# Optimization experiments

Hardware: AMD Instinct MI355X
Metric: run time of the kernel (lower is better)

Reference implementation:

```python
import jax, jax.numpy as jnp
import numpy as np

N = 20000       # nodes
E = 320000      # edges (before self-loops)
F_IN = 128
HID = 128
HEADS = 4
OUT_DIM = 2
B = 64          # graphs in batch
SLOPE = 0.2     # GATv2 leaky_relu negative slope (PyG default)


def _glorot(key, shape):
    fan_in, fan_out = shape[0], shape[1]
    limit = np.sqrt(6.0 / (fan_in + fan_out)).astype(np.float32)
    return jax.random.uniform(key, shape, jnp.float32, -limit, limit)


def setup_inputs() -> dict:
    key = jax.random.key(0)
    ks = jax.random.split(key, 24)
    inp = {
        'x': jax.random.normal(ks[0], (N, F_IN), jnp.float32),
        'edge_src': jax.random.randint(ks[1], (E,), 0, N),
        'edge_dst': jax.random.randint(ks[2], (E,), 0, N),
        'batch': jnp.sort(jax.random.randint(ks[3], (N,), 0, B)),
        # layer 1: in=F_IN, out=HEADS*HID, concat
        'Wl1': _glorot(ks[4], (F_IN, HEADS * HID)),
        'Wr1': _glorot(ks[5], (F_IN, HEADS * HID)),
        'bl1': jnp.zeros((HEADS * HID,), jnp.float32),
        'br1': jnp.zeros((HEADS * HID,), jnp.float32),
        'att1': _glorot(ks[6], (HEADS, HID)),
        'bias1': jnp.zeros((HEADS * HID,), jnp.float32),
        # layer 2: in=HEADS*HID, out=HEADS*HID, concat
        'Wl2': _glorot(ks[7], (HEADS * HID, HEADS * HID)),
        'Wr2': _glorot(ks[8], (HEADS * HID, HEADS * HID)),
        'bl2': jnp.zeros((HEADS * HID,), jnp.float32),
        'br2': jnp.zeros((HEADS * HID,), jnp.float32),
        'att2': _glorot(ks[9], (HEADS, HID)),
        'bias2': jnp.zeros((HEADS * HID,), jnp.float32),
        # layer 3: in=HEADS*HID, heads=1, concat=False -> out=HID
        'Wl3': _glorot(ks[10], (HEADS * HID, HID)),
        'Wr3': _glorot(ks[11], (HEADS * HID, HID)),
        'bl3': jnp.zeros((HID,), jnp.float32),
        'br3': jnp.zeros((HID,), jnp.float32),
        'att3': _glorot(ks[12], (1, HID)),
        'bias3': jnp.zeros((HID,), jnp.float32),
        # output MLP
        'W_mlp1': _glorot(ks[13], (HID, HID)),
        'b_mlp1': jnp.zeros((HID,), jnp.float32),
        'W_mlp2': _glorot(ks[14], (HID, OUT_DIM)),
        'b_mlp2': jnp.zeros((OUT_DIM,), jnp.float32),
    }
    return inp


def gatv2_layer(x, src, dst, Wl, Wr, bl, br, att, bias, concat):
    """PyG GATv2Conv (eval mode): alpha_ij = softmax_j over N(i) of a^T LeakyReLU(xl_j + xr_i)."""
    H, C = att.shape
    n = x.shape[0]
    xl = (x @ Wl + bl).reshape(n, H, C)   # source transform
    e = jax.nn.leaky_relu(xl[src] + (x @ Wr + br).reshape(n, H, C)[dst], SLOPE)  # [E,H,C]
    logits = jnp.einsum('ehc,hc->eh', e, att)                                    # [E,H]
    # segment softmax over destination node
    m = jax.ops.segment_max(logits, dst, num_segments=n)
    alpha = jnp.exp(logits - m[dst])
    denom = jax.ops.segment_sum(alpha, dst, num_segments=n)
    alpha = alpha / denom[dst]
    out = jax.ops.segment_sum(xl[src] * alpha[..., None], dst, num_segments=n)   # [N,H,C]
    out = out.reshape(n, H * C) if concat else out.mean(axis=1)
    return out + bias


def reference(x, edge_src, edge_dst, batch,
              Wl1, Wr1, bl1, br1, att1, bias1,
              Wl2, Wr2, bl2, br2, att2, bias2,
              Wl3, Wr3, bl3, br3, att3, bias3,
              W_mlp1, b_mlp1, W_mlp2, b_mlp2):
    n = x.shape[0]
    loop = jnp.arange(n, dtype=edge_src.dtype)
    src = jnp.concatenate([edge_src, loop])   # PyG add_self_loops=True
    dst = jnp.concatenate([edge_dst, loop])

    h = jax.nn.elu(gatv2_layer(x, src, dst, Wl1, Wr1, bl1, br1, att1, bias1, True))
    h = jax.nn.elu(gatv2_layer(h, src, dst, Wl2, Wr2, bl2, br2, att2, bias2, True))
    h = jax.nn.elu(gatv2_layer(h, src, dst, Wl3, Wr3, bl3, br3, att3, bias3, False))

    # global_mean_pool over graph ids
    counts = jnp.maximum(jax.ops.segment_sum(jnp.ones((n,), h.dtype), batch, num_segments=B), 1.0)
    pooled = jax.ops.segment_sum(h, batch, num_segments=B) / counts[:, None]

    hidden = jax.nn.relu(pooled @ W_mlp1 + b_mlp1)
    return hidden @ W_mlp2 + b_mlp2
```

## Files before the change

### kernel.cpp

```cpp
#include <hip/hip_runtime.h>
#include <math.h>


typedef __attribute__((ext_vector_type(4))) float f32x4;
typedef __attribute__((ext_vector_type(8))) _Float16 f16x8;
typedef __attribute__((ext_vector_type(4))) _Float16 f16x4;
typedef __attribute__((ext_vector_type(2))) _Float16 f16x2;

__device__ __forceinline__ float elu1(float x) {
    return (x > 0.f) ? x : (__expf(x) - 1.f);
}
__device__ __forceinline__ f16x2 pk_leaky(f16x2 s) {
    const f16x2 slope = {(_Float16)0.2f, (_Float16)0.2f};
    return __builtin_elementwise_max(s, s * slope);
}

__device__ __forceinline__ float dpp_sum16(float v) {
    int t;
    t = __builtin_amdgcn_mov_dpp(__float_as_int(v), 0xB1, 0xF, 0xF, true);
    v += __int_as_float(t);
    t = __builtin_amdgcn_mov_dpp(__float_as_int(v), 0x4E, 0xF, 0xF, true);
    v += __int_as_float(t);
    t = __builtin_amdgcn_mov_dpp(__float_as_int(v), 0x141, 0xF, 0xF, true);
    v += __int_as_float(t);
    t = __builtin_amdgcn_mov_dpp(__float_as_int(v), 0x140, 0xF, 0xF, true);
    v += __int_as_float(t);
    return v;
}

__global__ void zero32_kernel(int* __restrict__ p, int n) {
    int i = blockIdx.x * 256 + threadIdx.x;
    if (i < n) p[i] = 0;
}

__global__ void count_kernel(const int* __restrict__ dst, int* __restrict__ cnt,
                             int E, int N) {
    int e = blockIdx.x * 256 + threadIdx.x;
    if (e < E + N) {
        int d = (e < E) ? dst[e] : (e - E);
        atomicAdd(&cnt[d], 1);
    }
}

__global__ __launch_bounds__(256) void scan1_kernel(const int* __restrict__ cnt,
                                                    int* __restrict__ psum, int N) {
    __shared__ int red[256];
    int idx = blockIdx.x * 256 + threadIdx.x;
    red[threadIdx.x] = (idx < N) ? cnt[idx] : 0;
    __syncthreads();
    for (int s = 128; s > 0; s >>= 1) {
        if (threadIdx.x < s) red[threadIdx.x] += red[threadIdx.x + s];
        __syncthreads();
    }
    if (threadIdx.x == 0) psum[blockIdx.x] = red[0];
}
__global__ void scan2_kernel(int* __restrict__ psum, int nch) {
    if (threadIdx.x == 0) {
        int run = 0;
        for (int i = 0; i < nch; ++i) { int v = psum[i]; psum[i] = run; run += v; }
    }
}
__global__ __launch_bounds__(256) void scan3_kernel(const int* __restrict__ cnt,
                                                    const int* __restrict__ psum,
                                                    int* __restrict__ rowstart,
                                                    int* __restrict__ cursor, int N) {
    __shared__ int buf[256];
    int idx = blockIdx.x * 256 + threadIdx.x;
    int v = (idx < N) ? cnt[idx] : 0;
    buf[threadIdx.x] = v;
    __syncthreads();
    for (int off = 1; off < 256; off <<= 1) {
        int t = (threadIdx.x >= off) ? buf[threadIdx.x - off] : 0;
        __syncthreads();
        buf[threadIdx.x] += t;
        __syncthreads();
    }
    int excl = buf[threadIdx.x] - v + psum[blockIdx.x];
    if (idx < N) {
        rowstart[idx] = excl;
        cursor[idx]   = excl;
        if (idx == N - 1) rowstart[N] = excl + v;
    }
}

__global__ void scatter_kernel(const int* __restrict__ src, const int* __restrict__ dst,
                               int* __restrict__ cursor, int* __restrict__ csr_src,
                               int E, int N) {
    int e = blockIdx.x * 256 + threadIdx.x;
    if (e < E + N) {
        int d, s;
        if (e < E) { d = dst[e]; s = src[e]; }
        else       { d = e - E; s = e - E; }
        int pos = atomicAdd(&cursor[d], 1);
        csr_src[pos] = s;
    }
}

__global__ void boundary_kernel(const int* __restrict__ batch,
                                int* __restrict__ gstart, int N, int B) {
    int n = blockIdx.x * 256 + threadIdx.x;
    if (n > N) return;
    int cur  = (n < N) ? batch[n] : B;
    int prev = (n == 0) ? -1 : batch[n - 1];
    for (int g = prev + 1; g <= cur; ++g) gstart[g] = n;
}

__global__ void convA_kernel(const float* __restrict__ X, _Float16* __restrict__ A,
                             int n_valid, int n_total) {
    int i = (blockIdx.x * 256 + threadIdx.x) * 4;
    if (i >= n_total) return;
    float4 v = (i < n_valid) ? *(const float4*)(X + i) : make_float4(0.f, 0.f, 0.f, 0.f);
    f16x4 h;
    h.x = (_Float16)v.x; h.y = (_Float16)v.y;
    h.z = (_Float16)v.z; h.w = (_Float16)v.w;
    *(f16x4*)(A + i) = h;
}

__global__ __launch_bounds__(256) void convWT_kernel(
    const float* __restrict__ Wl, const float* __restrict__ Wr,
    _Float16* __restrict__ Bth, _Float16* __restrict__ Btl, int K, int Nh) {
    __shared__ float tile[32][33];
    int kb = blockIdx.x * 32;
    int nb = blockIdx.y * 32;
    int tx = threadIdx.x;
    int ty = threadIdx.y;
#pragma unroll
    for (int j = 0; j < 4; ++j) {
        int kk = kb + ty + j * 8;
        int nn = nb + tx;
        float v = (nn < Nh) ? Wl[(size_t)kk * Nh + nn]
                            : Wr[(size_t)kk * Nh + (nn - Nh)];
        tile[ty + j * 8][tx] = v;
    }
    __syncthreads();
#pragma unroll
    for (int j = 0; j < 4; ++j) {
        int nn = nb + ty + j * 8;
        int kk = kb + tx;
        float v = tile[tx][ty + j * 8];
        _Float16 h = (_Float16)v;
        Bth[(size_t)nn * K + kk] = h;
        Btl[(size_t)nn * K + kk] = (_Float16)(v - (float)h);
    }
}

#define SCW 132
__global__ __launch_bounds__(256, 1) void gemm_f16_kernel(
    const _Float16* __restrict__ A,
    const _Float16* __restrict__ Bh, const _Float16* __restrict__ Bl,
    const float* __restrict__ biasL, const float* __restrict__ biasR, int Nh_,
    _Float16* __restrict__ P, _Float16* __restrict__ Q, int K, int NT) {
    __shared__ __align__(16) char smem[49152];
    float* sC = (float*)(smem);

    const int tid  = threadIdx.x;
    const int lane = tid & 63;
    const int wv   = tid >> 6;
    const int wm   = wv & 1;
    const int wn   = wv >> 1;
    const int fm   = lane & 15;
    const int q    = lane >> 4;

    const int bi = blockIdx.x;
    const int kx = bi & 7;
    const int tt = bi >> 3;
    const int m0 = ((tt / NT) * 8 + kx) * 128;
    const int n0 = (tt % NT) * 128;

    const int r0  = lane >> 2;
    const int kco = (lane & 3) << 3;

    f32x4 acc[4][4];
#pragma unroll
    for (int i = 0; i < 4; ++i)
#pragma unroll
        for (int j = 0; j < 4; ++j) {
            acc[i][j].x = 0.f; acc[i][j].y = 0.f;
            acc[i][j].z = 0.f; acc[i][j].w = 0.f;
        }

    const int nIters = K >> 5;
    int cur = 0;
    {
        char* base = smem;
#pragma unroll
        for (int j = 0; j < 2; ++j) {
            int wc  = wv * 2 + j;
            int row = wc * 16 + r0;
            size_t ga = (size_t)(m0 + row) * K + kco;
            size_t gb = (size_t)(n0 + row) * K + kco;
            int lofs = wc * 1024;
            __builtin_amdgcn_global_load_lds(
                (const __attribute__((address_space(1))) void*)(A + ga),
                (__attribute__((address_space(3))) void*)(base + lofs), 16, 0, 0);
            __builtin_amdgcn_global_load_lds(
                (const __attribute__((address_space(1))) void*)(Bh + gb),
                (__attribute__((address_space(3))) void*)(base + 8192 + lofs), 16, 0, 0);
            __builtin_amdgcn_global_load_lds(
                (const __attribute__((address_space(1))) void*)(Bl + gb),
                (__attribute__((address_space(3))) void*)(base + 16384 + lofs), 16, 0, 0);
        }
    }
    for (int it = 0; it < nIters; ++it) {
        __syncthreads();
        if (it + 1 < nIters) {
            char* base = smem + (cur ^ 1) * 24576;
            int ks = (it + 1) << 5;
#pragma unroll
            for (int j = 0; j < 2; ++j) {
                int wc  = wv * 2 + j;
                int row = wc * 16 + r0;
                size_t ga = (size_t)(m0 + row) * K + ks + kco;
                size_t gb = (size_t)(n0 + row) * K + ks + kco;
                int lofs = wc * 1024;
                __builtin_amdgcn_global_load_lds(
                    (const __attribute__((address_space(1))) void*)(A + ga),
                    (__attribute__((address_space(3))) void*)(base + lofs), 16, 0, 0);
                __builtin_amdgcn_global_load_lds(
                    (const __attribute__((address_space(1))) void*)(Bh + gb),
                    (__attribute__((address_space(3))) void*)(base + 8192 + lofs), 16, 0, 0);
                __builtin_amdgcn_global_load_lds(
                    (const __attribute__((address_space(1))) void*)(Bl + gb),
                    (__attribute__((address_space(3))) void*)(base + 16384 + lofs), 16, 0, 0);
            }
        }

        _Float16* cA  = (_Float16*)(smem + cur * 24576);
        _Float16* cBh = (_Float16*)(smem + cur * 24576 + 8192);
        _Float16* cBl = (_Float16*)(smem + cur * 24576 + 16384);
        f16x8 ah[4];
#pragma unroll
        for (int mi = 0; mi < 4; ++mi)
            ah[mi] = *(const f16x8*)&cA[(wm * 64 + mi * 16 + fm) * 32 + q * 8];
#pragma unroll
        for (int ni = 0; ni < 4; ++ni) {
            int r = (wn * 64 + ni * 16 + fm) * 32 + q * 8;
            f16x8 bh = *(const f16x8*)&cBh[r];
            f16x8 bl = *(const f16x8*)&cBl[r];
#pragma unroll
            for (int mi = 0; mi < 4; ++mi) {
                acc[mi][ni] = __builtin_amdgcn_mfma_f32_16x16x32_f16(ah[mi], bh, acc[mi][ni], 0, 0, 0);
                acc[mi][ni] = __builtin_amdgcn_mfma_f32_16x16x32_f16(ah[mi], bl, acc[mi][ni], 0, 0, 0);
            }
        }
        cur ^= 1;
    }

    float bsv[4];
#pragma unroll
    for (int ni = 0; ni < 4; ++ni) {
        int col = n0 + wn * 64 + ni * 16 + fm;
        bsv[ni] = (col < Nh_) ? biasL[col] : biasR[col - Nh_];
    }

    _Float16* dstbase = (n0 < Nh_) ? P : Q;
    const int col0 = (n0 < Nh_) ? n0 : (n0 - Nh_);

#pragma unroll
    for (int c = 0; c < 2; ++c) {
        __syncthreads();
        if (wm == c) {
#pragma unroll
            for (int mi = 0; mi < 4; ++mi)
#pragma unroll
                for (int ni = 0; ni < 4; ++ni) {
                    int base = (mi * 16 + q * 4) * SCW + wn * 64 + ni * 16 + fm;
                    sC[base]           = acc[mi][ni].x + bsv[ni];
                    sC[base + SCW]     = acc[mi][ni].y + bsv[ni];
                    sC[base + 2 * SCW] = acc[mi][ni].z + bsv[ni];
                    sC[base + 3 * SCW] = acc[mi][ni].w + bsv[ni];
                }
        }
        __syncthreads();
#pragma unroll
        for (int j = 0; j < 8; ++j) {
            int flat = j * 256 + tid;
            int row  = flat >> 5;
            int col  = (flat & 31) * 4;
            f32x4 v = *(const f32x4*)(sC + row * SCW + col);
            f16x4 hv;
            hv.x = (_Float16)v.x; hv.y = (_Float16)v.y;
            hv.z = (_Float16)v.z; hv.w = (_Float16)v.w;
            *(f16x4*)(dstbase + (size_t)(m0 + c * 64 + row) * Nh_ + col0 + col) = hv;
        }
    }
}


__device__ __forceinline__ void edge4_one(
    int s, const _Float16* __restrict__ P, int c0,
    const f16x2* r2, const f16x2* t2, float& l_run, float* acc) {
    f16x8 h = *(const f16x8*)(P + ((size_t)s << 9) + c0);
    float p = 0.f;
#pragma unroll
    for (int k = 0; k < 4; ++k) {
        f16x2 a; a.x = h[2 * k]; a.y = h[2 * k + 1];
        p = __builtin_amdgcn_fdot2(pk_leaky(a + r2[k]), t2[k], p, false);
    }
    p = dpp_sum16(p);
    float w = __expf(p);
    l_run += w;
#pragma unroll
    for (int j = 0; j < 8; ++j)
        acc[j] = fmaf((float)h[j], w, acc[j]);
}

__global__ __launch_bounds__(256) void gat_edge4_kernel(
    const _Float16* __restrict__ P, const _Float16* __restrict__ Q,
    const float* __restrict__ att, const float* __restrict__ bias,
    const int* __restrict__ rowstart, const int* __restrict__ srcs,
    _Float16* __restrict__ H, int N) {
    int wv = threadIdx.x >> 6;
    int lane = threadIdx.x & 63;
    int n = blockIdx.x * 4 + wv;
    if (n >= N) return;
    int c0 = lane * 8;

    f16x8 rv = *(const f16x8*)(Q + (size_t)n * 512 + c0);
    f16x2 r2[4], t2[4];
#pragma unroll
    for (int k = 0; k < 4; ++k) {
        r2[k].x = rv[2 * k]; r2[k].y = rv[2 * k + 1];
        t2[k].x = (_Float16)att[c0 + 2 * k];
        t2[k].y = (_Float16)att[c0 + 2 * k + 1];
    }

    float acc[8];
#pragma unroll
    for (int j = 0; j < 8; ++j) acc[j] = 0.f;
    float l_run = 0.f;

    int beg = __builtin_amdgcn_readfirstlane(rowstart[n]);
    int end = __builtin_amdgcn_readfirstlane(rowstart[n + 1]);

    int i = beg;
    int s0 = srcs[i], s1 = srcs[i + 1], s2 = srcs[i + 2], s3 = srcs[i + 3];

    for (; i + 3 < end; ) {
        int f0 = srcs[i + 4], f1 = srcs[i + 5], f2 = srcs[i + 6], f3 = srcs[i + 7];
        int u0 = __builtin_amdgcn_readfirstlane(s0);
        int u1 = __builtin_amdgcn_readfirstlane(s1);
        int u2 = __builtin_amdgcn_readfirstlane(s2);
        int u3 = __builtin_amdgcn_readfirstlane(s3);
        f16x8 h0 = *(const f16x8*)(P + ((size_t)u0 << 9) + c0);
        f16x8 h1 = *(const f16x8*)(P + ((size_t)u1 << 9) + c0);
        f16x8 h2 = *(const f16x8*)(P + ((size_t)u2 << 9) + c0);
        f16x8 h3 = *(const f16x8*)(P + ((size_t)u3 << 9) + c0);
        float p0 = 0.f, p1 = 0.f, p2 = 0.f, p3 = 0.f;
#pragma unroll
        for (int k = 0; k < 4; ++k) {
            f16x2 a0; a0.x = h0[2 * k]; a0.y = h0[2 * k + 1];
            f16x2 a1; a1.x = h1[2 * k]; a1.y = h1[2 * k + 1];
            f16x2 a2; a2.x = h2[2 * k]; a2.y = h2[2 * k + 1];
            f16x2 a3; a3.x = h3[2 * k]; a3.y = h3[2 * k + 1];
            p0 = __builtin_amdgcn_fdot2(pk_leaky(a0 + r2[k]), t2[k], p0, false);
            p1 = __builtin_amdgcn_fdot2(pk_leaky(a1 + r2[k]), t2[k], p1, false);
            p2 = __builtin_amdgcn_fdot2(pk_leaky(a2 + r2[k]), t2[k], p2, false);
            p3 = __builtin_amdgcn_fdot2(pk_leaky(a3 + r2[k]), t2[k], p3, false);
        }
        p0 = dpp_sum16(p0);
        p1 = dpp_sum16(p1);
        p2 = dpp_sum16(p2);
        p3 = dpp_sum16(p3);
        float w0 = __expf(p0);
        float w1 = __expf(p1);
        float w2 = __expf(p2);
        float w3 = __expf(p3);
        l_run += (w0 + w1) + (w2 + w3);
#pragma unroll
        for (int j = 0; j < 8; ++j) {
            float a = fmaf((float)h0[j], w0, acc[j]);
            a = fmaf((float)h1[j], w1, a);
            a = fmaf((float)h2[j], w2, a);
            acc[j] = fmaf((float)h3[j], w3, a);
        }
        i += 4; s0 = f0; s1 = f1; s2 = f2; s3 = f3;
    }
    int rem = end - i;
    if (rem > 0) edge4_one(__builtin_amdgcn_readfirstlane(s0), P, c0, r2, t2, l_run, acc);
    if (rem > 1) edge4_one(__builtin_amdgcn_readfirstlane(s1), P, c0, r2, t2, l_run, acc);
    if (rem > 2) edge4_one(__builtin_amdgcn_readfirstlane(s2), P, c0, r2, t2, l_run, acc);

    float inv = 1.f / l_run;
    f16x8 oh;
#pragma unroll
    for (int j = 0; j < 8; ++j)
        oh[j] = (_Float16)elu1(acc[j] * inv + bias[c0 + j]);
    *(f16x8*)(H + (size_t)n * 512 + c0) = oh;
}

__global__ __launch_bounds__(256) void gat_edge1_kernel(
    const _Float16* __restrict__ P, const _Float16* __restrict__ Q,
    const float* __restrict__ att, const float* __restrict__ bias,
    const int* __restrict__ rowstart, const int* __restrict__ srcs,
    float* __restrict__ out, int N) {
    int wv = threadIdx.x >> 6;
    int lane = threadIdx.x & 63;
    int n = blockIdx.x * 4 + wv;
    if (n >= N) return;
    int qd = lane >> 4;
    int lq = lane & 15;
    int c0 = lq * 8;

    f16x8 rv = *(const f16x8*)(Q + (size_t)n * 128 + c0);
    f16x2 r2[4], t2[4];
#pragma unroll
    for (int k = 0; k < 4; ++k) {
        r2[k].x = rv[2 * k]; r2[k].y = rv[2 * k + 1];
        t2[k].x = (_Float16)att[c0 + 2 * k];
        t2[k].y = (_Float16)att[c0 + 2 * k + 1];
    }

    float acc[8];
#pragma unroll
    for (int j = 0; j < 8; ++j) acc[j] = 0.f;
    float l_run = 0.f;

    int beg = __builtin_amdgcn_readfirstlane(rowstart[n]);
    int end = __builtin_amdgcn_readfirstlane(rowstart[n + 1]);
    for (int e = beg + qd; e < end; e += 4) {
        int s = srcs[e];
        f16x8 hv = *(const f16x8*)(P + ((size_t)s << 7) + c0);
        float p = 0.f;
#pragma unroll
        for (int k = 0; k < 4; ++k) {
            f16x2 a; a.x = hv[2 * k]; a.y = hv[2 * k + 1];
            p = __builtin_amdgcn_fdot2(pk_leaky(a + r2[k]), t2[k], p, false);
        }
        p = dpp_sum16(p);
        float w = __expf(p);
        l_run += w;
#pragma unroll
        for (int j = 0; j < 8; ++j)
            acc[j] = fmaf((float)hv[j], w, acc[j]);
    }
    l_run += __shfl_xor(l_run, 16, 64);
    l_run += __shfl_xor(l_run, 32, 64);
#pragma unroll
    for (int j = 0; j < 8; ++j) {
        acc[j] += __shfl_xor(acc[j], 16, 64);
        acc[j] += __shfl_xor(acc[j], 32, 64);
    }
    float inv = 1.f / l_run;
    int cw = c0 + qd * 2;
    float2 w2;
    w2.x = elu1(acc[qd * 2]     * inv + bias[cw]);
    w2.y = elu1(acc[qd * 2 + 1] * inv + bias[cw + 1]);
    *(float2*)(out + (size_t)n * 128 + cw) = w2;
}

__global__ __launch_bounds__(256) void pool2_kernel(
    const float* __restrict__ h3, const int* __restrict__ gstart,
    float* __restrict__ pooled) {
    __shared__ float red[256];
    int g = blockIdx.x;
    int c = threadIdx.x & 127;
    int h = threadIdx.x >> 7;
    int gs = gstart[g], ge = gstart[g + 1];
    float s = 0.f;
    for (int n = gs + h; n < ge; n += 2) s += h3[(size_t)n * 128 + c];
    red[threadIdx.x] = s;
    __syncthreads();
    if (h == 0) {
        float tot = red[c] + red[c + 128];
        float cnt = fmaxf((float)(ge - gs), 1.f);
        pooled[g * 128 + c] = tot / cnt;
    }
}

__global__ __launch_bounds__(128) void mlp_kernel(
    const float* __restrict__ pooled,
    const float* __restrict__ W1, const float* __restrict__ b1,
    const float* __restrict__ W2, const float* __restrict__ b2,
    float* __restrict__ out) {
    __shared__ float pr[128];
    __shared__ float2 red[128];
    int g = blockIdx.x;
    int t = threadIdx.x;
    pr[t] = pooled[g * 128 + t];
    __syncthreads();
    float h = b1[t];
#pragma unroll 4
    for (int k = 0; k < 128; ++k) h = fmaf(pr[k], W1[k * 128 + t], h);
    h = fmaxf(h, 0.0f);
    red[t] = make_float2(h * W2[t * 2], h * W2[t * 2 + 1]);
    __syncthreads();
    for (int s = 64; s > 0; s >>= 1) {
        if (t < s) {
            red[t].x += red[t + s].x;
            red[t].y += red[t + s].y;
        }
        __syncthreads();
    }
    if (t == 0) {
        out[g * 2]     = red[0].x + b2[0];
        out[g * 2 + 1] = red[0].y + b2[1];
    }
}

extern "C" void kernel_launch(void* const* d_in, const int* in_sizes, int n_in,
                              void* d_out, int out_size, void* d_ws, size_t ws_size,
                              hipStream_t stream) {
    const float* x     = (const float*)d_in[0];
    const int*   esrc  = (const int*)d_in[1];
    const int*   edst  = (const int*)d_in[2];
    const int*   batch = (const int*)d_in[3];
    const float* Wl1   = (const float*)d_in[4];
    const float* Wr1   = (const float*)d_in[5];
    const float* bl1   = (const float*)d_in[6];
    const float* br1   = (const float*)d_in[7];
    const float* att1  = (const float*)d_in[8];
    const float* bias1 = (const float*)d_in[9];
    const float* Wl2   = (const float*)d_in[10];
    const float* Wr2   = (const float*)d_in[11];
    const float* bl2   = (const float*)d_in[12];
    const float* br2   = (const float*)d_in[13];
    const float* att2  = (const float*)d_in[14];
    const float* bias2 = (const float*)d_in[15];
    const float* Wl3   = (const float*)d_in[16];
    const float* Wr3   = (const float*)d_in[17];
    const float* bl3   = (const float*)d_in[18];
    const float* br3   = (const float*)d_in[19];
    const float* att3  = (const float*)d_in[20];
    const float* bias3 = (const float*)d_in[21];
    const float* Wm1   = (const float*)d_in[22];
    const float* bm1   = (const float*)d_in[23];
    const float* Wm2   = (const float*)d_in[24];
    const float* bm2   = (const float*)d_in[25];

    int N  = in_sizes[0] / 128;
    int E  = in_sizes[1];
    int ET = E + N;
    int B  = out_size / 2;
    const int Mp = 160 * 128;
    int nch = (N + 255) / 256;

    char* ws = (char*)d_ws;
    size_t off = 0;
    auto alloc = [&](size_t bytes) -> void* {
        void* p = ws + off;
        off += (bytes + 255) & ~(size_t)255;
        return p;
    };
    _Float16* P    = (_Float16*)alloc((size_t)Mp * 512 * 2);
    _Float16* Q    = (_Float16*)alloc((size_t)Mp * 512 * 2);
    _Float16* A1   = (_Float16*)alloc((size_t)Mp * 128 * 2);
    _Float16* Hb   = (_Float16*)alloc((size_t)Mp * 512 * 2);
    _Float16* Wth1 = (_Float16*)alloc((size_t)1024 * 128 * 2);
    _Float16* Wtl1 = (_Float16*)alloc((size_t)1024 * 128 * 2);
    _Float16* Wth2 = (_Float16*)alloc((size_t)1024 * 512 * 2);
    _Float16* Wtl2 = (_Float16*)alloc((size_t)1024 * 512 * 2);
    _Float16* Wth3 = (_Float16*)alloc((size_t)256 * 512 * 2);
    _Float16* Wtl3 = (_Float16*)alloc((size_t)256 * 512 * 2);
    float*    R3   = (float*)alloc((size_t)Mp * 128 * 4);
    int*    cnt      = (int*)alloc((size_t)N * 4);
    int*    psum     = (int*)alloc((size_t)(nch + 1) * 4);
    int*    rowstart = (int*)alloc((size_t)(N + 1) * 4);
    int*    cursor   = (int*)alloc((size_t)N * 4);
    int*    csr_src  = (int*)alloc((size_t)ET * 4 + 32);
    int*    gstart   = (int*)alloc((size_t)(B + 1) * 4);
    float*  pooled   = (float*)alloc((size_t)B * 128 * 4);
    (void)ws_size;

    zero32_kernel<<<(N + 255) / 256, 256, 0, stream>>>(cnt, N);

    count_kernel<<<(ET + 255) / 256, 256, 0, stream>>>(edst, cnt, E, N);
    scan1_kernel<<<nch, 256, 0, stream>>>(cnt, psum, N);
    scan2_kernel<<<1, 64, 0, stream>>>(psum, nch);
    scan3_kernel<<<nch, 256, 0, stream>>>(cnt, psum, rowstart, cursor, N);
    scatter_kernel<<<(ET + 255) / 256, 256, 0, stream>>>(esrc, edst, cursor, csr_src, E, N);
    boundary_kernel<<<(N + 256) / 256, 256, 0, stream>>>(batch, gstart, N, B);

    convWT_kernel<<<dim3(4, 32),  dim3(32, 8), 0, stream>>>(Wl1, Wr1, Wth1, Wtl1, 128, 512);
    convWT_kernel<<<dim3(16, 32), dim3(32, 8), 0, stream>>>(Wl2, Wr2, Wth2, Wtl2, 512, 512);
    convWT_kernel<<<dim3(16, 8),  dim3(32, 8), 0, stream>>>(Wl3, Wr3, Wth3, Wtl3, 512, 128);

    convA_kernel<<<((Mp * 128 / 4) + 255) / 256, 256, 0, stream>>>(x, A1, N * 128, Mp * 128);

    int eblocks = (N + 3) / 4;

    gemm_f16_kernel<<<160 * 8, 256, 0, stream>>>(A1, Wth1, Wtl1, bl1, br1, 512, P, Q, 128, 8);
    gat_edge4_kernel<<<eblocks, 256, 0, stream>>>(P, Q, att1, bias1, rowstart, csr_src, Hb, N);

    gemm_f16_kernel<<<160 * 8, 256, 0, stream>>>(Hb, Wth2, Wtl2, bl2, br2, 512, P, Q, 512, 8);
    gat_edge4_kernel<<<eblocks, 256, 0, stream>>>(P, Q, att2, bias2, rowstart, csr_src, Hb, N);

    gemm_f16_kernel<<<160 * 2, 256, 0, stream>>>(Hb, Wth3, Wtl3, bl3, br3, 128, P, Q, 512, 2);
    gat_edge1_kernel<<<eblocks, 256, 0, stream>>>(P, Q, att3, bias3, rowstart, csr_src, R3, N);

    pool2_kernel<<<B, 256, 0, stream>>>(R3, gstart, pooled);
    mlp_kernel<<<B, 128, 0, stream>>>(pooled, Wm1, bm1, Wm2, bm2, (float*)d_out);
}
```

Measured before the change: 412.2 us.

## Sort nodes by degree for edge kernels and swizzle GEMM LDS layout

```diff
diff --git a/kernel.cpp b/kernel.cpp
--- a/kernel.cpp
+++ b/kernel.cpp
@@ -105,6 +105,32 @@
     for (int g = prev + 1; g <= cur; ++g) gstart[g] = n;
 }
 
+__global__ void degcnt_kernel(const int* __restrict__ rowstart,
+                              int* __restrict__ dcnt, int N) {
+    int n = blockIdx.x * 256 + threadIdx.x;
+    if (n < N) {
+        int d = rowstart[n + 1] - rowstart[n];
+        d = d < 63 ? d : 63;
+        atomicAdd(&dcnt[d], 1);
+    }
+}
+__global__ void degoff_kernel(const int* __restrict__ dcnt, int* __restrict__ dcur) {
+    if (threadIdx.x == 0) {
+        int run = 0;
+        for (int d = 63; d >= 0; --d) { dcur[d] = run; run += dcnt[d]; }
+    }
+}
+__global__ void degscat_kernel(const int* __restrict__ rowstart,
+                               int* __restrict__ dcur, int* __restrict__ order, int N) {
+    int n = blockIdx.x * 256 + threadIdx.x;
+    if (n < N) {
+        int d = rowstart[n + 1] - rowstart[n];
+        d = d < 63 ? d : 63;
+        int pos = atomicAdd(&dcur[d], 1);
+        order[pos] = n;
+    }
+}
+
 __global__ void convA_kernel(const float* __restrict__ X, _Float16* __restrict__ A,
                              int n_valid, int n_total) {
     int i = (blockIdx.x * 256 + threadIdx.x) * 4;
@@ -160,6 +186,7 @@
     const int wn   = wv >> 1;
     const int fm   = lane & 15;
     const int q    = lane >> 4;
+    const int qa   = q ^ ((fm >> 1) & 3);
 
     const int bi = blockIdx.x;
     const int kx = bi & 7;
@@ -168,7 +195,7 @@
     const int n0 = (tt % NT) * 128;
 
     const int r0  = lane >> 2;
-    const int kco = (lane & 3) << 3;
+    const int kcs = (((lane & 3) ^ ((lane >> 3) & 3)) << 3);
 
     f32x4 acc[4][4];
 #pragma unroll
@@ -187,8 +214,8 @@
         for (int j = 0; j < 2; ++j) {
             int wc  = wv * 2 + j;
             int row = wc * 16 + r0;
-            size_t ga = (size_t)(m0 + row) * K + kco;
-            size_t gb = (size_t)(n0 + row) * K + kco;
+            size_t ga = (size_t)(m0 + row) * K + kcs;
+            size_t gb = (size_t)(n0 + row) * K + kcs;
             int lofs = wc * 1024;
             __builtin_amdgcn_global_load_lds(
                 (const __attribute__((address_space(1))) void*)(A + ga),
@@ -210,8 +237,8 @@
             for (int j = 0; j < 2; ++j) {
                 int wc  = wv * 2 + j;
                 int row = wc * 16 + r0;
-                size_t ga = (size_t)(m0 + row) * K + ks + kco;
-                size_t gb = (size_t)(n0 + row) * K + ks + kco;
+                size_t ga = (size_t)(m0 + row) * K + ks + kcs;
+                size_t gb = (size_t)(n0 + row) * K + ks + kcs;
                 int lofs = wc * 1024;
                 __builtin_amdgcn_global_load_lds(
                     (const __attribute__((address_space(1))) void*)(A + ga),
@@ -231,10 +258,10 @@
         f16x8 ah[4];
 #pragma unroll
         for (int mi = 0; mi < 4; ++mi)
-            ah[mi] = *(const f16x8*)&cA[(wm * 64 + mi * 16 + fm) * 32 + q * 8];
+            ah[mi] = *(const f16x8*)&cA[(wm * 64 + mi * 16 + fm) * 32 + qa * 8];
 #pragma unroll
         for (int ni = 0; ni < 4; ++ni) {
-            int r = (wn * 64 + ni * 16 + fm) * 32 + q * 8;
+            int r = (wn * 64 + ni * 16 + fm) * 32 + qa * 8;
             f16x8 bh = *(const f16x8*)&cBh[r];
             f16x8 bl = *(const f16x8*)&cBl[r];
 #pragma unroll
@@ -290,30 +317,31 @@
 __device__ __forceinline__ void edge4_one(
     int s, const _Float16* __restrict__ P, int c0,
     const f16x2* r2, const f16x2* t2, float& l_run, float* acc) {
-    f16x8 h = *(const f16x8*)(P + ((size_t)s << 9) + c0);
+    union { f16x8 v; f16x2 p[4]; } h;
+    h.v = *(const f16x8*)(P + ((size_t)s << 9) + c0);
     float p = 0.f;
 #pragma unroll
-    for (int k = 0; k < 4; ++k) {
-        f16x2 a; a.x = h[2 * k]; a.y = h[2 * k + 1];
-        p = __builtin_amdgcn_fdot2(pk_leaky(a + r2[k]), t2[k], p, false);
-    }
+    for (int k = 0; k < 4; ++k)
+        p = __builtin_amdgcn_fdot2(pk_leaky(h.p[k] + r2[k]), t2[k], p, false);
     p = dpp_sum16(p);
     float w = __expf(p);
     l_run += w;
 #pragma unroll
     for (int j = 0; j < 8; ++j)
-        acc[j] = fmaf((float)h[j], w, acc[j]);
+        acc[j] = fmaf((float)h.v[j], w, acc[j]);
 }
 
 __global__ __launch_bounds__(256) void gat_edge4_kernel(
     const _Float16* __restrict__ P, const _Float16* __restrict__ Q,
     const float* __restrict__ att, const float* __restrict__ bias,
     const int* __restrict__ rowstart, const int* __restrict__ srcs,
+    const int* __restrict__ order,
     _Float16* __restrict__ H, int N) {
     int wv = threadIdx.x >> 6;
     int lane = threadIdx.x & 63;
-    int n = blockIdx.x * 4 + wv;
-    if (n >= N) return;
+    int idx = blockIdx.x * 4 + wv;
+    if (idx >= N) return;
+    int n = order[idx];
     int c0 = lane * 8;
 
     f16x8 rv = *(const f16x8*)(Q + (size_t)n * 512 + c0);
@@ -342,21 +370,18 @@
         int u1 = __builtin_amdgcn_readfirstlane(s1);
         int u2 = __builtin_amdgcn_readfirstlane(s2);
         int u3 = __builtin_amdgcn_readfirstlane(s3);
-        f16x8 h0 = *(const f16x8*)(P + ((size_t)u0 << 9) + c0);
-        f16x8 h1 = *(const f16x8*)(P + ((size_t)u1 << 9) + c0);
-        f16x8 h2 = *(const f16x8*)(P + ((size_t)u2 << 9) + c0);
-        f16x8 h3 = *(const f16x8*)(P + ((size_t)u3 << 9) + c0);
+        union { f16x8 v; f16x2 p[4]; } h0, h1, h2, h3;
+        h0.v = *(const f16x8*)(P + ((size_t)u0 << 9) + c0);
+        h1.v = *(const f16x8*)(P + ((size_t)u1 << 9) + c0);
+        h2.v = *(const f16x8*)(P + ((size_t)u2 << 9) + c0);
+        h3.v = *(const f16x8*)(P + ((size_t)u3 << 9) + c0);
         float p0 = 0.f, p1 = 0.f, p2 = 0.f, p3 = 0.f;
 #pragma unroll
         for (int k = 0; k < 4; ++k) {
-            f16x2 a0; a0.x = h0[2 * k]; a0.y = h0[2 * k + 1];
-            f16x2 a1; a1.x = h1[2 * k]; a1.y = h1[2 * k + 1];
-            f16x2 a2; a2.x = h2[2 * k]; a2.y = h2[2 * k + 1];
-            f16x2 a3; a3.x = h3[2 * k]; a3.y = h3[2 * k + 1];
-            p0 = __builtin_amdgcn_fdot2(pk_leaky(a0 + r2[k]), t2[k], p0, false);
-            p1 = __builtin_amdgcn_fdot2(pk_leaky(a1 + r2[k]), t2[k], p1, false);
-            p2 = __builtin_amdgcn_fdot2(pk_leaky(a2 + r2[k]), t2[k], p2, false);
-            p3 = __builtin_amdgcn_fdot2(pk_leaky(a3 + r2[k]), t2[k], p3, false);
+            p0 = __builtin_amdgcn_fdot2(pk_leaky(h0.p[k] + r2[k]), t2[k], p0, false);
+            p1 = __builtin_amdgcn_fdot2(pk_leaky(h1.p[k] + r2[k]), t2[k], p1, false);
+            p2 = __builtin_amdgcn_fdot2(pk_leaky(h2.p[k] + r2[k]), t2[k], p2, false);
+            p3 = __builtin_amdgcn_fdot2(pk_leaky(h3.p[k] + r2[k]), t2[k], p3, false);
         }
         p0 = dpp_sum16(p0);
         p1 = dpp_sum16(p1);
@@ -369,10 +394,10 @@
         l_run += (w0 + w1) + (w2 + w3);
 #pragma unroll
         for (int j = 0; j < 8; ++j) {
-            float a = fmaf((float)h0[j], w0, acc[j]);
-            a = fmaf((float)h1[j], w1, a);
-            a = fmaf((float)h2[j], w2, a);
-            acc[j] = fmaf((float)h3[j], w3, a);
+            float a = fmaf((float)h0.v[j], w0, acc[j]);
+            a = fmaf((float)h1.v[j], w1, a);
+            a = fmaf((float)h2.v[j], w2, a);
+            acc[j] = fmaf((float)h3.v[j], w3, a);
         }
         i += 4; s0 = f0; s1 = f1; s2 = f2; s3 = f3;
     }
@@ -393,11 +418,13 @@
     const _Float16* __restrict__ P, const _Float16* __restrict__ Q,
     const float* __restrict__ att, const float* __restrict__ bias,
     const int* __restrict__ rowstart, const int* __restrict__ srcs,
+    const int* __restrict__ order,
     float* __restrict__ out, int N) {
     int wv = threadIdx.x >> 6;
     int lane = threadIdx.x & 63;
-    int n = blockIdx.x * 4 + wv;
-    if (n >= N) return;
+    int idx = blockIdx.x * 4 + wv;
+    if (idx >= N) return;
+    int n = order[idx];
     int qd = lane >> 4;
     int lq = lane & 15;
     int c0 = lq * 8;
@@ -420,19 +447,18 @@
     int end = __builtin_amdgcn_readfirstlane(rowstart[n + 1]);
     for (int e = beg + qd; e < end; e += 4) {
         int s = srcs[e];
-        f16x8 hv = *(const f16x8*)(P + ((size_t)s << 7) + c0);
+        union { f16x8 v; f16x2 p[4]; } hv;
+        hv.v = *(const f16x8*)(P + ((size_t)s << 7) + c0);
         float p = 0.f;
 #pragma unroll
-        for (int k = 0; k < 4; ++k) {
-            f16x2 a; a.x = hv[2 * k]; a.y = hv[2 * k + 1];
-            p = __builtin_amdgcn_fdot2(pk_leaky(a + r2[k]), t2[k], p, false);
-        }
+        for (int k = 0; k < 4; ++k)
+            p = __builtin_amdgcn_fdot2(pk_leaky(hv.p[k] + r2[k]), t2[k], p, false);
         p = dpp_sum16(p);
         float w = __expf(p);
         l_run += w;
 #pragma unroll
         for (int j = 0; j < 8; ++j)
-            acc[j] = fmaf((float)hv[j], w, acc[j]);
+            acc[j] = fmaf((float)hv.v[j], w, acc[j]);
     }
     l_run += __shfl_xor(l_run, 16, 64);
     l_run += __shfl_xor(l_run, 32, 64);
@@ -557,12 +583,16 @@
     int*    psum     = (int*)alloc((size_t)(nch + 1) * 4);
     int*    rowstart = (int*)alloc((size_t)(N + 1) * 4);
     int*    cursor   = (int*)alloc((size_t)N * 4);
-    int*    csr_src  = (int*)alloc((size_t)ET * 4 + 32);
+    int*    csr_src  = (int*)alloc((size_t)ET * 4 + 64);
     int*    gstart   = (int*)alloc((size_t)(B + 1) * 4);
     float*  pooled   = (float*)alloc((size_t)B * 128 * 4);
+    int*    dcnt     = (int*)alloc((size_t)64 * 4);
+    int*    dcur     = (int*)alloc((size_t)64 * 4);
+    int*    order    = (int*)alloc((size_t)N * 4 + 64);
     (void)ws_size;
 
     zero32_kernel<<<(N + 255) / 256, 256, 0, stream>>>(cnt, N);
+    zero32_kernel<<<1, 256, 0, stream>>>(dcnt, 64);
 
     count_kernel<<<(ET + 255) / 256, 256, 0, stream>>>(edst, cnt, E, N);
     scan1_kernel<<<nch, 256, 0, stream>>>(cnt, psum, N);
@@ -571,6 +601,10 @@
     scatter_kernel<<<(ET + 255) / 256, 256, 0, stream>>>(esrc, edst, cursor, csr_src, E, N);
     boundary_kernel<<<(N + 256) / 256, 256, 0, stream>>>(batch, gstart, N, B);
 
+    degcnt_kernel<<<(N + 255) / 256, 256, 0, stream>>>(rowstart, dcnt, N);
+    degoff_kernel<<<1, 64, 0, stream>>>(dcnt, dcur);
+    degscat_kernel<<<(N + 255) / 256, 256, 0, stream>>>(rowstart, dcur, order, N);
+
     convWT_kernel<<<dim3(4, 32),  dim3(32, 8), 0, stream>>>(Wl1, Wr1, Wth1, Wtl1, 128, 512);
     convWT_kernel<<<dim3(16, 32), dim3(32, 8), 0, stream>>>(Wl2, Wr2, Wth2, Wtl2, 512, 512);
     convWT_kernel<<<dim3(16, 8),  dim3(32, 8), 0, stream>>>(Wl3, Wr3, Wth3, Wtl3, 512, 128);
@@ -580,13 +614,13 @@
     int eblocks = (N + 3) / 4;
 
     gemm_f16_kernel<<<160 * 8, 256, 0, stream>>>(A1, Wth1, Wtl1, bl1, br1, 512, P, Q, 128, 8);
-    gat_edge4_kernel<<<eblocks, 256, 0, stream>>>(P, Q, att1, bias1, rowstart, csr_src, Hb, N);
+    gat_edge4_kernel<<<eblocks, 256, 0, stream>>>(P, Q, att1, bias1, rowstart, csr_src, order, Hb, N);
 
     gemm_f16_kernel<<<160 * 8, 256, 0, stream>>>(Hb, Wth2, Wtl2, bl2, br2, 512, P, Q, 512, 8);
-    gat_edge4_kernel<<<eblocks, 256, 0, stream>>>(P, Q, att2, bias2, rowstart, csr_src, Hb, N);
+    gat_edge4_kernel<<<eblocks, 256, 0, stream>>>(P, Q, att2, bias2, rowstart, csr_src, order, Hb, N);
 
     gemm_f16_kernel<<<160 * 2, 256, 0, stream>>>(Hb, Wth3, Wtl3, bl3, br3, 128, P, Q, 512, 2);
-    gat_edge1_kernel<<<eblocks, 256, 0, stream>>>(P, Q, att3, bias3, rowstart, csr_src, R3, N);
+    gat_edge1_kernel<<<eblocks, 256, 0, stream>>>(P, Q, att3, bias3, rowstart, csr_src, order, R3, N);
 
     pool2_kernel<<<B, 256, 0, stream>>>(R3, gstart, pooled);
     mlp_kernel<<<B, 128, 0, stream>>>(pooled, Wm1, bm1, Wm2, bm2, (float*)d_out);
```

Result: slower. 528.8 us (+28.3%).
